# Performance work log

Hardware: AMD Instinct MI355X
Metric: run time of the kernel (lower is better)

## Reference

```python
import jax, jax.numpy as jnp
import numpy as np

B, T, E, H = 2, 2048, 1024, 16
M1, M2 = 1024, 256
DH = E // H


def setup_inputs() -> dict:
    key = jax.random.key(0)
    ks = jax.random.split(key, 8)
    return {
        "x": jax.random.normal(ks[0], (B, T, E), dtype=jnp.float32),
        "K1": jax.random.normal(ks[1], (B, M1, E), dtype=jnp.float32),
        "V1": jax.random.normal(ks[2], (B, M1, E), dtype=jnp.float32),
        "K2": jax.random.normal(ks[3], (B, M2, E), dtype=jnp.float32),
        "V2": jax.random.normal(ks[4], (B, M2, E), dtype=jnp.float32),
        "Wq": jax.random.normal(ks[5], (E, E), dtype=jnp.float32) * (1.0 / np.sqrt(E)),
        "Wproj": jax.random.normal(ks[6], (E, E), dtype=jnp.float32) * (1.0 / np.sqrt(E)),
        "gate": jnp.asarray(-2.0, dtype=jnp.float32),
    }


def reference(x, K1, V1, K2, V2, Wq, Wproj, gate):
    Bx, Tx, Ex = x.shape
    dh = Ex // H
    scale = 1.0 / np.sqrt(dh).astype(np.float32)
    # Q: [B,T,H,dh]  (torch Linear: x @ W.T)
    Q = (x @ Wq.T).reshape(Bx, Tx, H, dh)

    def attend(Kf, Vf):
        M = Kf.shape[1]
        Kh = Kf.reshape(Bx, M, H, dh)
        Vh = Vf.reshape(Bx, M, H, dh)
        s = jnp.einsum("bthd,bmhd->bhtm", Q, Kh) * scale
        p = jax.nn.softmax(s, axis=-1)
        return jnp.einsum("bhtm,bmhd->bthd", p, Vh)

    ctx = attend(K1, V1) + attend(K2, V2)            # [B,T,H,dh]
    ctx = ctx.reshape(Bx, Tx, Ex) @ Wproj.T          # output projection
    alpha = jax.nn.sigmoid(gate)
    return alpha * ctx
```

## Files before the change

### kernel.cpp

```cpp
#include <hip/hip_runtime.h>

#define BB  2
#define TT  2048
#define EE  1024
#define HH  16
#define DH  64
#define MM1 1024
#define MM2 256

#define KSCL 0.18033688011112042f

typedef unsigned short u16;
typedef unsigned int   u32;
typedef __bf16 bf16x2 __attribute__((ext_vector_type(2)));
typedef __bf16 bf16x8 __attribute__((ext_vector_type(8)));
typedef float  f32x4  __attribute__((ext_vector_type(4)));

static __device__ __forceinline__ u32 f2bf_bits(float x) {
    union { float f; u32 u; } v; v.f = x;
    return (v.u + 0x7FFFu + ((v.u >> 16) & 1u)) >> 16;
}
static __device__ __forceinline__ u32 pkbf(float a, float b) {
    bf16x2 t; t.x = (__bf16)a; t.y = (__bf16)b;
    return __builtin_bit_cast(u32, t);
}
static __device__ __forceinline__ float fexp2(float x) {
    float r; asm("v_exp_f32 %0, %1" : "=v"(r) : "v"(x)); return r;
}
static __device__ __forceinline__ int swz(int row, int cb) {
    return row * 128 + (cb ^ ((row & 7) << 4));
}
static __device__ __forceinline__ void gload16(void* lds, const void* g) {
    __builtin_amdgcn_global_load_lds((const __attribute__((address_space(1))) u32*)g,
                                     (__attribute__((address_space(3))) u32*)lds, 16, 0, 0);
}

__global__ __launch_bounds__(256) void conv_all(const float* __restrict__ x,
                                                const float* __restrict__ wq,
                                                const float* __restrict__ wp,
                                                const float* __restrict__ K1, const float* __restrict__ V1,
                                                const float* __restrict__ K2, const float* __restrict__ V2,
                                                char* __restrict__ xs, char* __restrict__ wqs, char* __restrict__ wps,
                                                char* __restrict__ Kb1, char* __restrict__ Vb1,
                                                char* __restrict__ Kb2, char* __restrict__ Vb2)
{
    __shared__ u16 T[64 * 72];
    const int z = blockIdx.z, bx = blockIdx.x, by = blockIdx.y;
    const int tid = threadIdx.x;
    if (z < 3) {
        if (by >= 16) return;
        if (z > 0 && bx >= 8) return;
        const float* A = z == 0 ? x : (z == 1 ? wq : wp);
        char* Ab = z == 0 ? xs : (z == 1 ? wqs : wps);
        const int row = tid >> 1, half = tid & 1;
        const float* src = A + ((size_t)bx * 128 + row) * EE + by * 64 + half * 32;
        char* dst = Ab + ((size_t)(bx * 16 + by)) * 16384;
        float v[32];
        #pragma unroll
        for (int i = 0; i < 8; ++i) *(float4*)&v[i * 4] = ((const float4*)src)[i];
        u32 pk[16];
        #pragma unroll
        for (int j = 0; j < 16; ++j) pk[j] = pkbf(v[2 * j], v[2 * j + 1]);
        #pragma unroll
        for (int j = 0; j < 4; ++j)
            *(uint4*)(dst + swz(row, half * 64 + j * 16)) = *(uint4*)&pk[j * 4];
        return;
    }
    const int zz = z - 3;
    const int M = (zz >= 2) ? MM2 : MM1;
    if (bx * 64 >= M) return;
    const int isV = zz & 1;
    const float* src4[4] = { K1, V1, K2, V2 };
    char* dst4[4] = { Kb1, Vb1, Kb2, Vb2 };
    const int b = by >> 4, h = by & 15;
    char* dst = dst4[zz] + ((size_t)by * (M / 64) + bx) * 8192;
    const float* src = src4[zz] + ((size_t)b * M + (size_t)bx * 64) * EE + h * DH;
    const int m = tid >> 2, q = tid & 3;
    const float* s = src + (size_t)m * EE + q * 16;
    float v[16];
    #pragma unroll
    for (int i = 0; i < 4; ++i) *(float4*)&v[i * 4] = ((const float4*)s)[i];
    if (!isV) {
        u32 pk[8];
        #pragma unroll
        for (int j = 0; j < 8; ++j) pk[j] = pkbf(v[2 * j] * KSCL, v[2 * j + 1] * KSCL);
        *(uint4*)(dst + swz(m, q * 32))      = *(uint4*)&pk[0];
        *(uint4*)(dst + swz(m, q * 32 + 16)) = *(uint4*)&pk[4];
    } else {
        #pragma unroll
        for (int j = 0; j < 16; ++j) T[(q * 16 + j) * 72 + m] = (u16)f2bf_bits(v[j]);
        __syncthreads();
        const int d = tid >> 2, qq = tid & 3;
        uint4 a0 = *(const uint4*)((const char*)T + d * 144 + qq * 32);
        uint4 a1 = *(const uint4*)((const char*)T + d * 144 + qq * 32 + 16);
        *(uint4*)(dst + swz(d, qq * 32))      = a0;
        *(uint4*)(dst + swz(d, qq * 32 + 16)) = a1;
    }
}

template<bool FINAL>
__global__ __launch_bounds__(256) void gemm_swz(const char* __restrict__ Ab,
                                                const char* __restrict__ Bb,
                                                void* __restrict__ Cout,
                                                const float* __restrict__ gate)
{
    constexpr int NKT = EE / 64;
    __shared__ char As[2][16384];
    __shared__ char Bs[2][8192];
    const int tid = threadIdx.x, lane = tid & 63, w = tid >> 6;
    const int wr = w >> 1, wc = w & 1, g = lane >> 4, ln = lane & 15;
    int lin = blockIdx.y * 32 + blockIdx.x;
    lin = (lin & 7) * 64 + (lin >> 3);
    const int bmi = lin & 31, bni = lin >> 5;
    const char* Abase = Ab + (size_t)bmi * NKT * 16384;
    const char* Bbase = Bb + (size_t)(bni >> 1) * NKT * 16384 + (size_t)(bni & 1) * 8192;
    #pragma unroll
    for (int i = 0; i < 4; ++i) gload16(As[0] + tid * 16 + i * 4096, Abase + tid * 16 + i * 4096);
    #pragma unroll
    for (int i = 0; i < 2; ++i) gload16(Bs[0] + tid * 16 + i * 4096, Bbase + tid * 16 + i * 4096);
    f32x4 acc[4][2] = {};
    for (int kt = 0; kt < NKT; ++kt) {
        const int cur = kt & 1;
        __syncthreads();
        if (kt + 1 < NKT) {
            #pragma unroll
            for (int i = 0; i < 4; ++i)
                gload16(As[cur ^ 1] + tid * 16 + i * 4096,
                        Abase + (size_t)(kt + 1) * 16384 + tid * 16 + i * 4096);
            #pragma unroll
            for (int i = 0; i < 2; ++i)
                gload16(Bs[cur ^ 1] + tid * 16 + i * 4096,
                        Bbase + (size_t)(kt + 1) * 16384 + tid * 16 + i * 4096);
        }
        #pragma unroll
        for (int kh = 0; kh < 2; ++kh) {
            bf16x8 af[4], bf2[2];
            #pragma unroll
            for (int f = 0; f < 4; ++f)
                af[f] = *(const bf16x8*)(As[cur] + swz(wr * 64 + f * 16 + ln, kh * 64 + g * 16));
            #pragma unroll
            for (int j = 0; j < 2; ++j)
                bf2[j] = *(const bf16x8*)(Bs[cur] + swz(wc * 32 + j * 16 + ln, kh * 64 + g * 16));
            #pragma unroll
            for (int i = 0; i < 4; ++i)
                #pragma unroll
                for (int j = 0; j < 2; ++j)
                    acc[i][j] = __builtin_amdgcn_mfma_f32_16x16x32_bf16(af[i], bf2[j], acc[i][j], 0, 0, 0);
        }
    }
    float alpha = 1.0f;
    if constexpr (FINAL) alpha = 1.0f / (1.0f + __expf(-gate[0]));
    #pragma unroll
    for (int i = 0; i < 4; ++i)
        #pragma unroll
        for (int r = 0; r < 4; ++r) {
            const int row = bmi * 128 + wr * 64 + i * 16 + g * 4 + r;
            #pragma unroll
            for (int j = 0; j < 2; ++j) {
                const int col = bni * 64 + wc * 32 + j * 16 + ln;
                if constexpr (FINAL) ((float*)Cout)[(size_t)row * EE + col] = acc[i][j][r] * alpha;
                else ((u16*)Cout)[(size_t)row * EE + col] = (u16)f2bf_bits(acc[i][j][r]);
            }
        }
}

__global__ __launch_bounds__(256) void attn2(const u16* __restrict__ Qb,
                                             const char* __restrict__ Kb1, const char* __restrict__ Vb1,
                                             const char* __restrict__ Kb2, const char* __restrict__ Vb2,
                                             char* __restrict__ Ctxs)
{
    __shared__ char Ks[2][8192];
    __shared__ char Ps[4][4096];
    const int tid = threadIdx.x, lane = tid & 63, w = tid >> 6;
    const int g = lane >> 4, ln = lane & 15;
    const int lnx = (ln & 7) << 4;
    int lin = blockIdx.y * 16 + blockIdx.x;
    lin = (lin & 7) * 64 + (lin >> 3);
    const int bx = lin & 15, bh = lin >> 4;
    const int b = bh >> 4, h = bh & 15;
    const int t0 = bx * 128;
    constexpr int NT1 = MM1 / 64, NT = NT1 + MM2 / 64;

    bf16x8 qf[2][2];
    #pragma unroll
    for (int fr = 0; fr < 2; ++fr)
        #pragma unroll
        for (int kh = 0; kh < 2; ++kh)
            qf[fr][kh] = *(const bf16x8*)(Qb + ((size_t)(b * TT + t0 + w * 32 + fr * 16 + ln)) * EE
                                          + h * DH + kh * 32 + g * 8);

    const char* Kbase[2] = { Kb1 + (size_t)bh * (MM1 / 64) * 8192, Kb2 + (size_t)bh * (MM2 / 64) * 8192 };
    const char* Vbase[2] = { Vb1 + (size_t)bh * (MM1 / 64) * 8192, Vb2 + (size_t)bh * (MM2 / 64) * 8192 };

    gload16(Ks[0] + tid * 16,        Kbase[0] + tid * 16);
    gload16(Ks[0] + tid * 16 + 4096, Kbase[0] + tid * 16 + 4096);

    f32x4 oacc[2][4] = {}, outacc[2][4] = {};
    float psum[2] = {};

    for (int ti = 0; ti < NT; ++ti) {
        const int cur = ti & 1;
        const int pi = (ti >= NT1) ? 1 : 0, mt = pi ? ti - NT1 : ti;
        const char* vt = Vbase[pi] + (size_t)mt * 8192;
        __syncthreads();
        bf16x8 vf[2][4];
        #pragma unroll
        for (int ks = 0; ks < 2; ++ks)
            #pragma unroll
            for (int f = 0; f < 4; ++f)
                vf[ks][f] = *(const bf16x8*)(vt + swz(f * 16 + ln, ks * 64 + g * 16));
        __builtin_amdgcn_sched_barrier(0);
        if (ti + 1 < NT) {
            const int nx = ti + 1;
            const int pn = (nx >= NT1) ? 1 : 0, mtn = pn ? nx - NT1 : nx;
            const char* kn = Kbase[pn] + (size_t)mtn * 8192;
            gload16(Ks[cur ^ 1] + tid * 16,        kn + tid * 16);
            gload16(Ks[cur ^ 1] + tid * 16 + 4096, kn + tid * 16 + 4096);
        }
        f32x4 s[2][4] = {};
        __builtin_amdgcn_s_setprio(1);
        #pragma unroll
        for (int kh = 0; kh < 2; ++kh)
            #pragma unroll
            for (int f = 0; f < 4; ++f) {
                const bf16x8 kf = *(const bf16x8*)(Ks[cur] + swz(f * 16 + ln, kh * 64 + g * 16));
                s[0][f] = __builtin_amdgcn_mfma_f32_16x16x32_bf16(kf, qf[0][kh], s[0][f], 0, 0, 0);
                s[1][f] = __builtin_amdgcn_mfma_f32_16x16x32_bf16(kf, qf[1][kh], s[1][f], 0, 0, 0);
            }
        __builtin_amdgcn_s_setprio(0);
        #pragma unroll
        for (int fr = 0; fr < 2; ++fr)
            #pragma unroll
            for (int f = 0; f < 4; ++f) {
                const float p0 = fexp2(s[fr][f][0]);
                const float p1 = fexp2(s[fr][f][1]);
                const float p2 = fexp2(s[fr][f][2]);
                const float p3 = fexp2(s[fr][f][3]);
                psum[fr] += (p0 + p1) + (p2 + p3);
                uint2 w2; w2.x = pkbf(p0, p1); w2.y = pkbf(p2, p3);
                *(uint2*)(Ps[w] + (fr * 16 + ln) * 128 + ((f * 32 + g * 8) ^ lnx)) = w2;
            }
        __builtin_amdgcn_s_setprio(1);
        #pragma unroll
        for (int ks = 0; ks < 2; ++ks) {
            const bf16x8 pf0 = *(const bf16x8*)(Ps[w] + ln * 128 + ((ks * 64 + g * 16) ^ lnx));
            const bf16x8 pf1 = *(const bf16x8*)(Ps[w] + (16 + ln) * 128 + ((ks * 64 + g * 16) ^ lnx));
            #pragma unroll
            for (int f = 0; f < 4; ++f) {
                oacc[0][f] = __builtin_amdgcn_mfma_f32_16x16x32_bf16(vf[ks][f], pf0, oacc[0][f], 0, 0, 0);
                oacc[1][f] = __builtin_amdgcn_mfma_f32_16x16x32_bf16(vf[ks][f], pf1, oacc[1][f], 0, 0, 0);
            }
        }
        __builtin_amdgcn_s_setprio(0);
        if (ti == NT1 - 1 || ti == NT - 1) {
            #pragma unroll
            for (int fr = 0; fr < 2; ++fr) {
                float t = psum[fr];
                t += __shfl_xor(t, 16);
                t += __shfl_xor(t, 32);
                const float inv = 1.0f / t;
                #pragma unroll
                for (int f = 0; f < 4; ++f)
                    #pragma unroll
                    for (int r = 0; r < 4; ++r) {
                        outacc[fr][f][r] += oacc[fr][f][r] * inv;
                        oacc[fr][f][r] = 0.0f;
                    }
                psum[fr] = 0.0f;
            }
        }
    }

    __syncthreads();
    char* eb = &Ks[0][0];
    #pragma unroll
    for (int fr = 0; fr < 2; ++fr)
        #pragma unroll
        for (int f = 0; f < 4; ++f) {
            uint2 w2;
            w2.x = pkbf(outacc[fr][f][0], outacc[fr][f][1]);
            w2.y = pkbf(outacc[fr][f][2], outacc[fr][f][3]);
            *(uint2*)(eb + (w * 32 + fr * 16 + ln) * 128 + ((f * 32 + g * 8) ^ lnx)) = w2;
        }
    __syncthreads();
    char* blob = Ctxs + ((size_t)((b * 16 + bx) * 16 + h)) * 16384;
    #pragma unroll
    for (int i = 0; i < 4; ++i)
        *(uint4*)(blob + tid * 16 + i * 4096) = *(const uint4*)(eb + tid * 16 + i * 4096);
}

extern "C" void kernel_launch(void* const* d_in, const int* in_sizes, int n_in,
                              void* d_out, int out_size, void* d_ws, size_t ws_size,
                              hipStream_t stream) {
    const float* x    = (const float*)d_in[0];
    const float* K1   = (const float*)d_in[1];
    const float* V1   = (const float*)d_in[2];
    const float* K2   = (const float*)d_in[3];
    const float* V2   = (const float*)d_in[4];
    const float* Wq   = (const float*)d_in[5];
    const float* Wp   = (const float*)d_in[6];
    const float* gate = (const float*)d_in[7];
    float* out = (float*)d_out;

    char* ws  = (char*)d_ws;
    char* Xs  = ws;
    char* Wqs = ws + (8u  << 20);
    char* Wps = ws + (10u << 20);
    u16*  Qb  = (u16*)(ws + (12u << 20));
    char* Kb1 = ws + (20u << 20);
    char* Vb1 = ws + (24u << 20);
    char* Kb2 = ws + (28u << 20);
    char* Vb2 = ws + (29u << 20);

    dim3 blk(256);
    conv_all<<<dim3(32, 32, 7), blk, 0, stream>>>(x, Wq, Wp, K1, V1, K2, V2,
                                                  Xs, Wqs, Wps, Kb1, Vb1, Kb2, Vb2);
    gemm_swz<false><<<dim3(32, 16), blk, 0, stream>>>(Xs, Wqs, Qb, nullptr);
    attn2<<<dim3(16, 32), blk, 0, stream>>>(Qb, Kb1, Vb1, Kb2, Vb2, Xs );
    gemm_swz<true><<<dim3(32, 16), blk, 0, stream>>>(Xs, Wps, out, gate);
}
```

Baseline: 99.50 us.

## Split attention block across eight waves and stage V tiles in LDS

The attention kernel now runs 512 threads per block, with each wave handling 16 query rows instead of 32. This halves per-wave register use and Q/accumulator state. V tiles are now double-buffered in shared memory alongside K via async loads, replacing the per-iteration direct global reads of V. The aim is more latency hiding and less exposed global load latency. The cost is twice as many LDS reads of K and V per block, because each wave now issues MFMAs with only one query fragment per K/V fragment.

```diff
diff --git a/kernel.cpp b/kernel.cpp
--- a/kernel.cpp
+++ b/kernel.cpp
@@ -164,13 +164,13 @@
         }
 }
 
-__global__ __launch_bounds__(256) void attn2(const u16* __restrict__ Qb,
+__global__ __launch_bounds__(512) void attn2(const u16* __restrict__ Qb,
                                              const char* __restrict__ Kb1, const char* __restrict__ Vb1,
                                              const char* __restrict__ Kb2, const char* __restrict__ Vb2,
                                              char* __restrict__ Ctxs)
 {
-    __shared__ char Ks[2][8192];
-    __shared__ char Ps[4][4096];
+    __shared__ char KV[2][16384];
+    __shared__ char Ps[8][2048];
     const int tid = threadIdx.x, lane = tid & 63, w = tid >> 6;
     const int g = lane >> 4, ln = lane & 15;
     const int lnx = (ln & 7) << 4;
@@ -181,112 +181,91 @@
     const int t0 = bx * 128;
     constexpr int NT1 = MM1 / 64, NT = NT1 + MM2 / 64;
 
-    bf16x8 qf[2][2];
-    #pragma unroll
-    for (int fr = 0; fr < 2; ++fr)
-        #pragma unroll
-        for (int kh = 0; kh < 2; ++kh)
-            qf[fr][kh] = *(const bf16x8*)(Qb + ((size_t)(b * TT + t0 + w * 32 + fr * 16 + ln)) * EE
-                                          + h * DH + kh * 32 + g * 8);
+    bf16x8 qf[2];
+    #pragma unroll
+    for (int kh = 0; kh < 2; ++kh)
+        qf[kh] = *(const bf16x8*)(Qb + ((size_t)(b * TT + t0 + w * 16 + ln)) * EE
+                                  + h * DH + kh * 32 + g * 8);
 
     const char* Kbase[2] = { Kb1 + (size_t)bh * (MM1 / 64) * 8192, Kb2 + (size_t)bh * (MM2 / 64) * 8192 };
     const char* Vbase[2] = { Vb1 + (size_t)bh * (MM1 / 64) * 8192, Vb2 + (size_t)bh * (MM2 / 64) * 8192 };
 
-    gload16(Ks[0] + tid * 16,        Kbase[0] + tid * 16);
-    gload16(Ks[0] + tid * 16 + 4096, Kbase[0] + tid * 16 + 4096);
-
-    f32x4 oacc[2][4] = {}, outacc[2][4] = {};
-    float psum[2] = {};
+    gload16(KV[0] + tid * 16,        Kbase[0] + tid * 16);
+    gload16(KV[0] + 8192 + tid * 16, Vbase[0] + tid * 16);
+
+    f32x4 oacc[4] = {}, outacc[4] = {};
+    float psum = 0.0f;
 
     for (int ti = 0; ti < NT; ++ti) {
         const int cur = ti & 1;
-        const int pi = (ti >= NT1) ? 1 : 0, mt = pi ? ti - NT1 : ti;
-        const char* vt = Vbase[pi] + (size_t)mt * 8192;
         __syncthreads();
-        bf16x8 vf[2][4];
-        #pragma unroll
-        for (int ks = 0; ks < 2; ++ks)
-            #pragma unroll
-            for (int f = 0; f < 4; ++f)
-                vf[ks][f] = *(const bf16x8*)(vt + swz(f * 16 + ln, ks * 64 + g * 16));
-        __builtin_amdgcn_sched_barrier(0);
         if (ti + 1 < NT) {
             const int nx = ti + 1;
             const int pn = (nx >= NT1) ? 1 : 0, mtn = pn ? nx - NT1 : nx;
-            const char* kn = Kbase[pn] + (size_t)mtn * 8192;
-            gload16(Ks[cur ^ 1] + tid * 16,        kn + tid * 16);
-            gload16(Ks[cur ^ 1] + tid * 16 + 4096, kn + tid * 16 + 4096);
-        }
-        f32x4 s[2][4] = {};
+            gload16(KV[cur ^ 1] + tid * 16,        Kbase[pn] + (size_t)mtn * 8192 + tid * 16);
+            gload16(KV[cur ^ 1] + 8192 + tid * 16, Vbase[pn] + (size_t)mtn * 8192 + tid * 16);
+        }
+        f32x4 s[4] = {};
         __builtin_amdgcn_s_setprio(1);
         #pragma unroll
         for (int kh = 0; kh < 2; ++kh)
             #pragma unroll
             for (int f = 0; f < 4; ++f) {
-                const bf16x8 kf = *(const bf16x8*)(Ks[cur] + swz(f * 16 + ln, kh * 64 + g * 16));
-                s[0][f] = __builtin_amdgcn_mfma_f32_16x16x32_bf16(kf, qf[0][kh], s[0][f], 0, 0, 0);
-                s[1][f] = __builtin_amdgcn_mfma_f32_16x16x32_bf16(kf, qf[1][kh], s[1][f], 0, 0, 0);
+                const bf16x8 kf = *(const bf16x8*)(KV[cur] + swz(f * 16 + ln, kh * 64 + g * 16));
+                s[f] = __builtin_amdgcn_mfma_f32_16x16x32_bf16(kf, qf[kh], s[f], 0, 0, 0);
             }
         __builtin_amdgcn_s_setprio(0);
         #pragma unroll
-        for (int fr = 0; fr < 2; ++fr)
+        for (int f = 0; f < 4; ++f) {
+            const float p0 = fexp2(s[f][0]);
+            const float p1 = fexp2(s[f][1]);
+            const float p2 = fexp2(s[f][2]);
+            const float p3 = fexp2(s[f][3]);
+            psum += (p0 + p1) + (p2 + p3);
+            uint2 w2; w2.x = pkbf(p0, p1); w2.y = pkbf(p2, p3);
+            *(uint2*)(Ps[w] + ln * 128 + ((f * 32 + g * 8) ^ lnx)) = w2;
+        }
+        __builtin_amdgcn_s_setprio(1);
+        #pragma unroll
+        for (int ks = 0; ks < 2; ++ks) {
+            const bf16x8 pf = *(const bf16x8*)(Ps[w] + ln * 128 + ((ks * 64 + g * 16) ^ lnx));
             #pragma unroll
             for (int f = 0; f < 4; ++f) {
-                const float p0 = fexp2(s[fr][f][0]);
-                const float p1 = fexp2(s[fr][f][1]);
-                const float p2 = fexp2(s[fr][f][2]);
-                const float p3 = fexp2(s[fr][f][3]);
-                psum[fr] += (p0 + p1) + (p2 + p3);
-                uint2 w2; w2.x = pkbf(p0, p1); w2.y = pkbf(p2, p3);
-                *(uint2*)(Ps[w] + (fr * 16 + ln) * 128 + ((f * 32 + g * 8) ^ lnx)) = w2;
-            }
-        __builtin_amdgcn_s_setprio(1);
-        #pragma unroll
-        for (int ks = 0; ks < 2; ++ks) {
-            const bf16x8 pf0 = *(const bf16x8*)(Ps[w] + ln * 128 + ((ks * 64 + g * 16) ^ lnx));
-            const bf16x8 pf1 = *(const bf16x8*)(Ps[w] + (16 + ln) * 128 + ((ks * 64 + g * 16) ^ lnx));
-            #pragma unroll
-            for (int f = 0; f < 4; ++f) {
-                oacc[0][f] = __builtin_amdgcn_mfma_f32_16x16x32_bf16(vf[ks][f], pf0, oacc[0][f], 0, 0, 0);
-                oacc[1][f] = __builtin_amdgcn_mfma_f32_16x16x32_bf16(vf[ks][f], pf1, oacc[1][f], 0, 0, 0);
+                const bf16x8 vf = *(const bf16x8*)(KV[cur] + 8192 + swz(f * 16 + ln, ks * 64 + g * 16));
+                oacc[f] = __builtin_amdgcn_mfma_f32_16x16x32_bf16(vf, pf, oacc[f], 0, 0, 0);
             }
         }
         __builtin_amdgcn_s_setprio(0);
         if (ti == NT1 - 1 || ti == NT - 1) {
-            #pragma unroll
-            for (int fr = 0; fr < 2; ++fr) {
-                float t = psum[fr];
-                t += __shfl_xor(t, 16);
-                t += __shfl_xor(t, 32);
-                const float inv = 1.0f / t;
+            float t = psum;
+            t += __shfl_xor(t, 16);
+            t += __shfl_xor(t, 32);
+            const float inv = 1.0f / t;
+            #pragma unroll
+            for (int f = 0; f < 4; ++f)
                 #pragma unroll
-                for (int f = 0; f < 4; ++f)
-                    #pragma unroll
-                    for (int r = 0; r < 4; ++r) {
-                        outacc[fr][f][r] += oacc[fr][f][r] * inv;
-                        oacc[fr][f][r] = 0.0f;
-                    }
-                psum[fr] = 0.0f;
-            }
+                for (int r = 0; r < 4; ++r) {
+                    outacc[f][r] += oacc[f][r] * inv;
+                    oacc[f][r] = 0.0f;
+                }
+            psum = 0.0f;
         }
     }
 
     __syncthreads();
-    char* eb = &Ks[0][0];
-    #pragma unroll
-    for (int fr = 0; fr < 2; ++fr)
-        #pragma unroll
-        for (int f = 0; f < 4; ++f) {
-            uint2 w2;
-            w2.x = pkbf(outacc[fr][f][0], outacc[fr][f][1]);
-            w2.y = pkbf(outacc[fr][f][2], outacc[fr][f][3]);
-            *(uint2*)(eb + (w * 32 + fr * 16 + ln) * 128 + ((f * 32 + g * 8) ^ lnx)) = w2;
-        }
+    char* eb = &KV[0][0];
+    #pragma unroll
+    for (int f = 0; f < 4; ++f) {
+        uint2 w2;
+        w2.x = pkbf(outacc[f][0], outacc[f][1]);
+        w2.y = pkbf(outacc[f][2], outacc[f][3]);
+        *(uint2*)(eb + (w * 16 + ln) * 128 + ((f * 32 + g * 8) ^ lnx)) = w2;
+    }
     __syncthreads();
     char* blob = Ctxs + ((size_t)((b * 16 + bx) * 16 + h)) * 16384;
     #pragma unroll
-    for (int i = 0; i < 4; ++i)
-        *(uint4*)(blob + tid * 16 + i * 4096) = *(const uint4*)(eb + tid * 16 + i * 4096);
+    for (int i = 0; i < 2; ++i)
+        *(uint4*)(blob + tid * 16 + i * 8192) = *(const uint4*)(eb + tid * 16 + i * 8192);
 }
 
 extern "C" void kernel_launch(void* const* d_in, const int* in_sizes, int n_in,
@@ -316,6 +295,6 @@
     conv_all<<<dim3(32, 32, 7), blk, 0, stream>>>(x, Wq, Wp, K1, V1, K2, V2,
                                                   Xs, Wqs, Wps, Kb1, Vb1, Kb2, Vb2);
     gemm_swz<false><<<dim3(32, 16), blk, 0, stream>>>(Xs, Wqs, Qb, nullptr);
-    attn2<<<dim3(16, 32), blk, 0, stream>>>(Qb, Kb1, Vb1, Kb2, Vb2, Xs );
+    attn2<<<dim3(16, 32), dim3(512), 0, stream>>>(Qb, Kb1, Vb1, Kb2, Vb2, Xs );
     gemm_swz<true><<<dim3(32, 16), blk, 0, stream>>>(Xs, Wps, out, gate);
 }
```

Result: faster. 93.34 us (-6.2%).

## Split attention KV tiles across two wave groups with 512-thread blocks

Applied to the files above, without the earlier changes.

The attention kernel moves to 512 threads per block. Two groups of four waves each handle half of every 64-key tile, and their partial outputs and row sums are merged through LDS at the end of each memory pass. V tiles are now staged into LDS alongside K through async loads, instead of being read per wave straight from global memory. The aim is more waves per CU for latency hiding and less redundant global V traffic. The cost is extra barriers, an LDS reduction, and bf16-packed accumulation of the two attention results, which adds some rounding.

```diff
diff --git a/kernel.cpp b/kernel.cpp
--- a/kernel.cpp
+++ b/kernel.cpp
@@ -23,6 +23,12 @@
 static __device__ __forceinline__ u32 pkbf(float a, float b) {
     bf16x2 t; t.x = (__bf16)a; t.y = (__bf16)b;
     return __builtin_bit_cast(u32, t);
+}
+static __device__ __forceinline__ float bflo(u32 v) {
+    union { u32 u; float f; } t; t.u = v << 16; return t.f;
+}
+static __device__ __forceinline__ float bfhi(u32 v) {
+    union { u32 u; float f; } t; t.u = v & 0xffff0000u; return t.f;
 }
 static __device__ __forceinline__ float fexp2(float x) {
     float r; asm("v_exp_f32 %0, %1" : "=v"(r) : "v"(x)); return r;
@@ -164,14 +170,15 @@
         }
 }
 
-__global__ __launch_bounds__(256) void attn2(const u16* __restrict__ Qb,
-                                             const char* __restrict__ Kb1, const char* __restrict__ Vb1,
-                                             const char* __restrict__ Kb2, const char* __restrict__ Vb2,
-                                             char* __restrict__ Ctxs)
+__global__ __launch_bounds__(512, 4) void attn4(const u16* __restrict__ Qb,
+                                                const char* __restrict__ Kb1, const char* __restrict__ Vb1,
+                                                const char* __restrict__ Kb2, const char* __restrict__ Vb2,
+                                                char* __restrict__ Ctxs)
 {
-    __shared__ char Ks[2][8192];
-    __shared__ char Ps[4][4096];
+    __shared__ char KV[2][16384];
+    __shared__ char PS[8 * 2560];
     const int tid = threadIdx.x, lane = tid & 63, w = tid >> 6;
+    const int w4 = w & 3, mh = w >> 2;
     const int g = lane >> 4, ln = lane & 15;
     const int lnx = (ln & 7) << 4;
     int lin = blockIdx.y * 16 + blockIdx.x;
@@ -186,44 +193,36 @@
     for (int fr = 0; fr < 2; ++fr)
         #pragma unroll
         for (int kh = 0; kh < 2; ++kh)
-            qf[fr][kh] = *(const bf16x8*)(Qb + ((size_t)(b * TT + t0 + w * 32 + fr * 16 + ln)) * EE
+            qf[fr][kh] = *(const bf16x8*)(Qb + ((size_t)(b * TT + t0 + w4 * 32 + fr * 16 + ln)) * EE
                                           + h * DH + kh * 32 + g * 8);
 
     const char* Kbase[2] = { Kb1 + (size_t)bh * (MM1 / 64) * 8192, Kb2 + (size_t)bh * (MM2 / 64) * 8192 };
     const char* Vbase[2] = { Vb1 + (size_t)bh * (MM1 / 64) * 8192, Vb2 + (size_t)bh * (MM2 / 64) * 8192 };
 
-    gload16(Ks[0] + tid * 16,        Kbase[0] + tid * 16);
-    gload16(Ks[0] + tid * 16 + 4096, Kbase[0] + tid * 16 + 4096);
-
-    f32x4 oacc[2][4] = {}, outacc[2][4] = {};
+    gload16(KV[0] + tid * 16,        Kbase[0] + tid * 16);
+    gload16(KV[0] + 8192 + tid * 16, Vbase[0] + tid * 16);
+
+    char* Pw = PS + w * 2560;
+    f32x4 oacc[2][4] = {};
+    u32 outp[2][4][2] = {};
     float psum[2] = {};
 
     for (int ti = 0; ti < NT; ++ti) {
         const int cur = ti & 1;
-        const int pi = (ti >= NT1) ? 1 : 0, mt = pi ? ti - NT1 : ti;
-        const char* vt = Vbase[pi] + (size_t)mt * 8192;
         __syncthreads();
-        bf16x8 vf[2][4];
-        #pragma unroll
-        for (int ks = 0; ks < 2; ++ks)
-            #pragma unroll
-            for (int f = 0; f < 4; ++f)
-                vf[ks][f] = *(const bf16x8*)(vt + swz(f * 16 + ln, ks * 64 + g * 16));
-        __builtin_amdgcn_sched_barrier(0);
         if (ti + 1 < NT) {
             const int nx = ti + 1;
             const int pn = (nx >= NT1) ? 1 : 0, mtn = pn ? nx - NT1 : nx;
-            const char* kn = Kbase[pn] + (size_t)mtn * 8192;
-            gload16(Ks[cur ^ 1] + tid * 16,        kn + tid * 16);
-            gload16(Ks[cur ^ 1] + tid * 16 + 4096, kn + tid * 16 + 4096);
-        }
-        f32x4 s[2][4] = {};
+            gload16(KV[cur ^ 1] + tid * 16,        Kbase[pn] + (size_t)mtn * 8192 + tid * 16);
+            gload16(KV[cur ^ 1] + 8192 + tid * 16, Vbase[pn] + (size_t)mtn * 8192 + tid * 16);
+        }
+        f32x4 s[2][2] = {};
         __builtin_amdgcn_s_setprio(1);
         #pragma unroll
         for (int kh = 0; kh < 2; ++kh)
             #pragma unroll
-            for (int f = 0; f < 4; ++f) {
-                const bf16x8 kf = *(const bf16x8*)(Ks[cur] + swz(f * 16 + ln, kh * 64 + g * 16));
+            for (int f = 0; f < 2; ++f) {
+                const bf16x8 kf = *(const bf16x8*)(KV[cur] + swz(mh * 32 + f * 16 + ln, kh * 64 + g * 16));
                 s[0][f] = __builtin_amdgcn_mfma_f32_16x16x32_bf16(kf, qf[0][kh], s[0][f], 0, 0, 0);
                 s[1][f] = __builtin_amdgcn_mfma_f32_16x16x32_bf16(kf, qf[1][kh], s[1][f], 0, 0, 0);
             }
@@ -231,62 +230,88 @@
         #pragma unroll
         for (int fr = 0; fr < 2; ++fr)
             #pragma unroll
-            for (int f = 0; f < 4; ++f) {
+            for (int f = 0; f < 2; ++f) {
                 const float p0 = fexp2(s[fr][f][0]);
                 const float p1 = fexp2(s[fr][f][1]);
                 const float p2 = fexp2(s[fr][f][2]);
                 const float p3 = fexp2(s[fr][f][3]);
                 psum[fr] += (p0 + p1) + (p2 + p3);
                 uint2 w2; w2.x = pkbf(p0, p1); w2.y = pkbf(p2, p3);
-                *(uint2*)(Ps[w] + (fr * 16 + ln) * 128 + ((f * 32 + g * 8) ^ lnx)) = w2;
-            }
+                *(uint2*)(Pw + (fr * 16 + ln) * 80 + f * 32 + g * 8) = w2;
+            }
+        bf16x8 vf[4];
+        #pragma unroll
+        for (int f2 = 0; f2 < 4; ++f2)
+            vf[f2] = *(const bf16x8*)(KV[cur] + 8192 + swz(f2 * 16 + ln, mh * 64 + g * 16));
         __builtin_amdgcn_s_setprio(1);
         #pragma unroll
-        for (int ks = 0; ks < 2; ++ks) {
-            const bf16x8 pf0 = *(const bf16x8*)(Ps[w] + ln * 128 + ((ks * 64 + g * 16) ^ lnx));
-            const bf16x8 pf1 = *(const bf16x8*)(Ps[w] + (16 + ln) * 128 + ((ks * 64 + g * 16) ^ lnx));
-            #pragma unroll
-            for (int f = 0; f < 4; ++f) {
-                oacc[0][f] = __builtin_amdgcn_mfma_f32_16x16x32_bf16(vf[ks][f], pf0, oacc[0][f], 0, 0, 0);
-                oacc[1][f] = __builtin_amdgcn_mfma_f32_16x16x32_bf16(vf[ks][f], pf1, oacc[1][f], 0, 0, 0);
-            }
+        for (int fr = 0; fr < 2; ++fr) {
+            const bf16x8 pf = *(const bf16x8*)(Pw + (fr * 16 + ln) * 80 + g * 16);
+            #pragma unroll
+            for (int f2 = 0; f2 < 4; ++f2)
+                oacc[fr][f2] = __builtin_amdgcn_mfma_f32_16x16x32_bf16(vf[f2], pf, oacc[fr][f2], 0, 0, 0);
         }
         __builtin_amdgcn_s_setprio(0);
         if (ti == NT1 - 1 || ti == NT - 1) {
             #pragma unroll
             for (int fr = 0; fr < 2; ++fr) {
-                float t = psum[fr];
-                t += __shfl_xor(t, 16);
-                t += __shfl_xor(t, 32);
-                const float inv = 1.0f / t;
+                __syncthreads();
+                if (mh == 1) {
+                    float4* dst = (float4*)(PS + (w4 * 64 + lane) * 64);
+                    #pragma unroll
+                    for (int f2 = 0; f2 < 4; ++f2) {
+                        float4 t4; t4.x = oacc[fr][f2][0]; t4.y = oacc[fr][f2][1];
+                        t4.z = oacc[fr][f2][2]; t4.w = oacc[fr][f2][3];
+                        dst[f2] = t4;
+                    }
+                    *(float*)(PS + 16384 + (w4 * 64 + lane) * 4) = psum[fr];
+                }
+                __syncthreads();
+                if (mh == 0) {
+                    const float4* src = (const float4*)(PS + (w4 * 64 + lane) * 64);
+                    float tot = psum[fr] + *(const float*)(PS + 16384 + (w4 * 64 + lane) * 4);
+                    tot += __shfl_xor(tot, 16);
+                    tot += __shfl_xor(tot, 32);
+                    const float inv = 1.0f / tot;
+                    #pragma unroll
+                    for (int f2 = 0; f2 < 4; ++f2) {
+                        const float4 s4 = src[f2];
+                        const float v0 = (oacc[fr][f2][0] + s4.x) * inv;
+                        const float v1 = (oacc[fr][f2][1] + s4.y) * inv;
+                        const float v2 = (oacc[fr][f2][2] + s4.z) * inv;
+                        const float v3 = (oacc[fr][f2][3] + s4.w) * inv;
+                        const u32 p0 = outp[fr][f2][0], p1 = outp[fr][f2][1];
+                        outp[fr][f2][0] = pkbf(bflo(p0) + v0, bfhi(p0) + v1);
+                        outp[fr][f2][1] = pkbf(bflo(p1) + v2, bfhi(p1) + v3);
+                    }
+                }
                 #pragma unroll
-                for (int f = 0; f < 4; ++f)
+                for (int f2 = 0; f2 < 4; ++f2)
                     #pragma unroll
-                    for (int r = 0; r < 4; ++r) {
-                        outacc[fr][f][r] += oacc[fr][f][r] * inv;
-                        oacc[fr][f][r] = 0.0f;
-                    }
+                    for (int r = 0; r < 4; ++r) oacc[fr][f2][r] = 0.0f;
                 psum[fr] = 0.0f;
             }
         }
     }
 
     __syncthreads();
-    char* eb = &Ks[0][0];
-    #pragma unroll
-    for (int fr = 0; fr < 2; ++fr)
-        #pragma unroll
-        for (int f = 0; f < 4; ++f) {
-            uint2 w2;
-            w2.x = pkbf(outacc[fr][f][0], outacc[fr][f][1]);
-            w2.y = pkbf(outacc[fr][f][2], outacc[fr][f][3]);
-            *(uint2*)(eb + (w * 32 + fr * 16 + ln) * 128 + ((f * 32 + g * 8) ^ lnx)) = w2;
-        }
+    char* eb = &KV[0][0];
+    if (mh == 0) {
+        #pragma unroll
+        for (int fr = 0; fr < 2; ++fr) {
+            const int row = w4 * 32 + fr * 16 + ln;
+            #pragma unroll
+            for (int f2 = 0; f2 < 4; ++f2) {
+                uint2 w2; w2.x = outp[fr][f2][0]; w2.y = outp[fr][f2][1];
+                *(uint2*)(eb + row * 128 + ((f2 * 32 + g * 8) ^ lnx)) = w2;
+            }
+        }
+    }
     __syncthreads();
     char* blob = Ctxs + ((size_t)((b * 16 + bx) * 16 + h)) * 16384;
     #pragma unroll
-    for (int i = 0; i < 4; ++i)
-        *(uint4*)(blob + tid * 16 + i * 4096) = *(const uint4*)(eb + tid * 16 + i * 4096);
+    for (int i = 0; i < 2; ++i)
+        *(uint4*)(blob + tid * 16 + i * 8192) = *(const uint4*)(eb + tid * 16 + i * 8192);
 }
 
 extern "C" void kernel_launch(void* const* d_in, const int* in_sizes, int n_in,
@@ -316,6 +341,6 @@
     conv_all<<<dim3(32, 32, 7), blk, 0, stream>>>(x, Wq, Wp, K1, V1, K2, V2,
                                                   Xs, Wqs, Wps, Kb1, Vb1, Kb2, Vb2);
     gemm_swz<false><<<dim3(32, 16), blk, 0, stream>>>(Xs, Wqs, Qb, nullptr);
-    attn2<<<dim3(16, 32), blk, 0, stream>>>(Qb, Kb1, Vb1, Kb2, Vb2, Xs );
+    attn4<<<dim3(16, 32), dim3(512), 0, stream>>>(Qb, Kb1, Vb1, Kb2, Vb2, Xs );
     gemm_swz<true><<<dim3(32, 16), blk, 0, stream>>>(Xs, Wps, out, gate);
 }
```

New measurement: 95.80 us. 1.04x faster.

## Stage V through LDS and double query rows per attention block

Applied to the files above, without the earlier changes.

The attention kernel now uses 512-thread blocks covering 256 query rows each. Both K and V tiles are double-buffered in shared memory, so V is no longer read directly from global memory by every wave. This increases reuse of each K/V tile across more query rows and removes per-wave global V loads from the critical path. The costs are higher LDS usage per block and fewer, larger blocks in the grid.

```diff
diff --git a/kernel.cpp b/kernel.cpp
--- a/kernel.cpp
+++ b/kernel.cpp
@@ -164,21 +164,21 @@
         }
 }
 
-__global__ __launch_bounds__(256) void attn2(const u16* __restrict__ Qb,
-                                             const char* __restrict__ Kb1, const char* __restrict__ Vb1,
-                                             const char* __restrict__ Kb2, const char* __restrict__ Vb2,
-                                             char* __restrict__ Ctxs)
+__global__ __launch_bounds__(512, 2) void attn5(const u16* __restrict__ Qb,
+                                                const char* __restrict__ Kb1, const char* __restrict__ Vb1,
+                                                const char* __restrict__ Kb2, const char* __restrict__ Vb2,
+                                                char* __restrict__ Ctxs)
 {
-    __shared__ char Ks[2][8192];
-    __shared__ char Ps[4][4096];
+    __shared__ char KV[2][16384];
+    __shared__ char Ps[8][4096];
     const int tid = threadIdx.x, lane = tid & 63, w = tid >> 6;
     const int g = lane >> 4, ln = lane & 15;
     const int lnx = (ln & 7) << 4;
-    int lin = blockIdx.y * 16 + blockIdx.x;
-    lin = (lin & 7) * 64 + (lin >> 3);
-    const int bx = lin & 15, bh = lin >> 4;
+    int lin = blockIdx.y * 8 + blockIdx.x;
+    lin = (lin & 7) * 32 + (lin >> 3);
+    const int bx = lin & 7, bh = lin >> 3;
     const int b = bh >> 4, h = bh & 15;
-    const int t0 = bx * 128;
+    const int t0 = bx * 256;
     constexpr int NT1 = MM1 / 64, NT = NT1 + MM2 / 64;
 
     bf16x8 qf[2][2];
@@ -192,30 +192,20 @@
     const char* Kbase[2] = { Kb1 + (size_t)bh * (MM1 / 64) * 8192, Kb2 + (size_t)bh * (MM2 / 64) * 8192 };
     const char* Vbase[2] = { Vb1 + (size_t)bh * (MM1 / 64) * 8192, Vb2 + (size_t)bh * (MM2 / 64) * 8192 };
 
-    gload16(Ks[0] + tid * 16,        Kbase[0] + tid * 16);
-    gload16(Ks[0] + tid * 16 + 4096, Kbase[0] + tid * 16 + 4096);
+    gload16(KV[0] + tid * 16,        Kbase[0] + tid * 16);
+    gload16(KV[0] + 8192 + tid * 16, Vbase[0] + tid * 16);
 
     f32x4 oacc[2][4] = {}, outacc[2][4] = {};
     float psum[2] = {};
 
     for (int ti = 0; ti < NT; ++ti) {
         const int cur = ti & 1;
-        const int pi = (ti >= NT1) ? 1 : 0, mt = pi ? ti - NT1 : ti;
-        const char* vt = Vbase[pi] + (size_t)mt * 8192;
         __syncthreads();
-        bf16x8 vf[2][4];
-        #pragma unroll
-        for (int ks = 0; ks < 2; ++ks)
-            #pragma unroll
-            for (int f = 0; f < 4; ++f)
-                vf[ks][f] = *(const bf16x8*)(vt + swz(f * 16 + ln, ks * 64 + g * 16));
-        __builtin_amdgcn_sched_barrier(0);
         if (ti + 1 < NT) {
             const int nx = ti + 1;
             const int pn = (nx >= NT1) ? 1 : 0, mtn = pn ? nx - NT1 : nx;
-            const char* kn = Kbase[pn] + (size_t)mtn * 8192;
-            gload16(Ks[cur ^ 1] + tid * 16,        kn + tid * 16);
-            gload16(Ks[cur ^ 1] + tid * 16 + 4096, kn + tid * 16 + 4096);
+            gload16(KV[cur ^ 1] + tid * 16,        Kbase[pn] + (size_t)mtn * 8192 + tid * 16);
+            gload16(KV[cur ^ 1] + 8192 + tid * 16, Vbase[pn] + (size_t)mtn * 8192 + tid * 16);
         }
         f32x4 s[2][4] = {};
         __builtin_amdgcn_s_setprio(1);
@@ -223,7 +213,7 @@
         for (int kh = 0; kh < 2; ++kh)
             #pragma unroll
             for (int f = 0; f < 4; ++f) {
-                const bf16x8 kf = *(const bf16x8*)(Ks[cur] + swz(f * 16 + ln, kh * 64 + g * 16));
+                const bf16x8 kf = *(const bf16x8*)(KV[cur] + swz(f * 16 + ln, kh * 64 + g * 16));
                 s[0][f] = __builtin_amdgcn_mfma_f32_16x16x32_bf16(kf, qf[0][kh], s[0][f], 0, 0, 0);
                 s[1][f] = __builtin_amdgcn_mfma_f32_16x16x32_bf16(kf, qf[1][kh], s[1][f], 0, 0, 0);
             }
@@ -240,6 +230,12 @@
                 uint2 w2; w2.x = pkbf(p0, p1); w2.y = pkbf(p2, p3);
                 *(uint2*)(Ps[w] + (fr * 16 + ln) * 128 + ((f * 32 + g * 8) ^ lnx)) = w2;
             }
+        bf16x8 vf[2][4];
+        #pragma unroll
+        for (int ks = 0; ks < 2; ++ks)
+            #pragma unroll
+            for (int f = 0; f < 4; ++f)
+                vf[ks][f] = *(const bf16x8*)(KV[cur] + 8192 + swz(f * 16 + ln, ks * 64 + g * 16));
         __builtin_amdgcn_s_setprio(1);
         #pragma unroll
         for (int ks = 0; ks < 2; ++ks) {
@@ -272,7 +268,7 @@
     }
 
     __syncthreads();
-    char* eb = &Ks[0][0];
+    char* eb = &KV[0][0];
     #pragma unroll
     for (int fr = 0; fr < 2; ++fr)
         #pragma unroll
@@ -283,10 +279,16 @@
             *(uint2*)(eb + (w * 32 + fr * 16 + ln) * 128 + ((f * 32 + g * 8) ^ lnx)) = w2;
         }
     __syncthreads();
-    char* blob = Ctxs + ((size_t)((b * 16 + bx) * 16 + h)) * 16384;
-    #pragma unroll
-    for (int i = 0; i < 4; ++i)
-        *(uint4*)(blob + tid * 16 + i * 4096) = *(const uint4*)(eb + tid * 16 + i * 4096);
+    {
+        char* blob0 = Ctxs + ((size_t)((b * 16 + bx * 2) * 16 + h)) * 16384;
+        char* blob1 = Ctxs + ((size_t)((b * 16 + bx * 2 + 1) * 16 + h)) * 16384;
+        #pragma unroll
+        for (int i = 0; i < 4; ++i) {
+            const int off = tid * 16 + i * 8192;
+            char* dst = (off < 16384) ? (blob0 + off) : (blob1 + off - 16384);
+            *(uint4*)dst = *(const uint4*)(eb + off);
+        }
+    }
 }
 
 extern "C" void kernel_launch(void* const* d_in, const int* in_sizes, int n_in,
@@ -316,6 +318,6 @@
     conv_all<<<dim3(32, 32, 7), blk, 0, stream>>>(x, Wq, Wp, K1, V1, K2, V2,
                                                   Xs, Wqs, Wps, Kb1, Vb1, Kb2, Vb2);
     gemm_swz<false><<<dim3(32, 16), blk, 0, stream>>>(Xs, Wqs, Qb, nullptr);
-    attn2<<<dim3(16, 32), blk, 0, stream>>>(Qb, Kb1, Vb1, Kb2, Vb2, Xs );
+    attn5<<<dim3(8, 32), dim3(512), 0, stream>>>(Qb, Kb1, Vb1, Kb2, Vb2, Xs );
     gemm_swz<true><<<dim3(32, 16), blk, 0, stream>>>(Xs, Wps, out, gate);
 }
```

New measurement: 96.39 us. 1.03x faster.
